# Optimization experiments

Hardware: AMD Instinct MI355X
Metric: run time of the kernel (lower is better)

Reference implementation:

```python
import jax, jax.numpy as jnp
import numpy as np

N_NODES = 100000
DEG = 16          # regular-graph degree so degrees[start] > 0 for all nodes
STEPS = 32
D_FEAT = 16
MAXI32 = 2147483647


def setup_inputs() -> dict:
    key = jax.random.key(0)
    k1, k2, k3 = jax.random.split(key, 3)
    x = jax.random.normal(k1, (N_NODES, D_FEAT), dtype=jnp.float32)
    # CSR-style flat adjacency list: node v's neighbors are
    # adj_nodes[adj_offset[v] : adj_offset[v] + degrees[v]]
    adj_nodes = jax.random.randint(k2, (N_NODES * DEG,), 0, N_NODES, dtype=jnp.int32)
    adj_offset = (jnp.arange(N_NODES, dtype=jnp.int32) * DEG)
    degrees = jnp.full((N_NODES,), DEG, dtype=jnp.int32)
    # cache of random integers, one per (step, walk), as in the torch code
    choices = jax.random.randint(k3, (STEPS, N_NODES), 0, MAXI32, dtype=jnp.int32)
    return {"x": x, "adj_nodes": adj_nodes, "adj_offset": adj_offset,
            "degrees": degrees, "choices": choices}


def reference(x, adj_nodes, adj_offset, degrees, choices):
    """Non-backtracking random walk (Walker.sample_walks with start_p=1.0,
    all nodes having degree > 0, so start = arange(n)).
    Returns walks [steps+1, w] and walk_edges [steps, w]."""
    n = degrees.shape[0]
    nb_degrees = jnp.maximum(degrees - 1, 1)  # reduced degree for non-backtrack rewrite
    start = jnp.arange(n, dtype=jnp.int32)

    def step(carry, ch):
        prev, cur = carry                      # [w] previous / current nodes
        deg = degrees[cur]
        edge_idx = ch % deg                    # unweighted modulo edge choice
        chosen = adj_offset[cur] + edge_idx
        new = adj_nodes[chosen]
        bt = new == prev                       # backtracking walks
        # conditional rewrite: pick a different outgoing edge
        alt = adj_offset[cur] + (edge_idx + 1 + ch % nb_degrees[cur]) % deg
        chosen = jnp.where(bt, alt, chosen)
        new = jnp.where(bt, adj_nodes[alt], new)
        return (cur, new), (new, chosen)

    # prev = -1 at step 0 => bt is all-False, matching the i > 0 guard
    prev0 = jnp.full_like(start, -1)
    _, (nodes, walk_edges) = jax.lax.scan(step, (prev0, start), choices)
    walks = jnp.concatenate([start[None, :], nodes], axis=0)  # [steps+1, w]
    return walks, walk_edges
```

## Files before the change

### kernel.cpp

```cpp
#include <hip/hip_runtime.h>
#include <hip/hip_bf16.h>


#define DEG 16
#define CHAINS 2

__global__ void pack_check_kernel(const int* __restrict__ adj_nodes,
                                  const int* __restrict__ adj_offset,
                                  const int* __restrict__ degrees,
                                  int n,
                                  unsigned int* __restrict__ pk32,
                                  int* __restrict__ flag) {
    int v = blockIdx.x * blockDim.x + threadIdx.x;
    if (v >= n) return;

    bool bad = (degrees[v] != DEG) || (adj_offset[v] != v * DEG);

    const uint4* row4 = (const uint4*)(adj_nodes + (size_t)v * DEG);
    uint4 r[4];
    r[0] = row4[0]; r[1] = row4[1]; r[2] = row4[2]; r[3] = row4[3];
    const unsigned* rr = (const unsigned*)r;

    unsigned wv[8];
    unsigned hbits = 0;
#pragma unroll
    for (int j = 0; j < 8; ++j) {
        unsigned u0 = rr[2 * j];
        unsigned u1 = rr[2 * j + 1];
        if (u0 >= 131072u || u1 >= 131072u) bad = true;
        wv[j] = (u0 & 0xffffu) | ((u1 & 0xffffu) << 16);
        hbits |= ((u0 >> 16) & 1u) << (2 * j);
        hbits |= ((u1 >> 16) & 1u) << (2 * j + 1);
    }
    unsigned int* dst = pk32 + (size_t)v * 9;
#pragma unroll
    for (int j = 0; j < 8; ++j) dst[j] = wv[j];
    dst[8] = hbits;

    if (bad) atomicOr(flag, 1);
}

template <int STEPS>
__global__ __launch_bounds__(64) void walker_fast2(
    const unsigned short* __restrict__ pk,
    const int* __restrict__ choices,
    int* __restrict__ out, int n, int h,
    const int* __restrict__ flag,
    const int* __restrict__ adj_nodes,
    const int* __restrict__ adj_offset,
    const int* __restrict__ degrees) {

    int t = blockIdx.x * blockDim.x + threadIdx.x;
    if (t >= h) return;

    int* walks      = out;
    int* walk_edges = out + (STEPS + 1) * n;

    int w0 = t;
    int w1 = t + h;
    bool has1 = (w1 < n);
    int w1s = has1 ? w1 : w0;

    __builtin_nontemporal_store(w0, &walks[w0]);
    if (has1) __builtin_nontemporal_store(w1, &walks[w1]);

    if (*flag == 0) {
        int c0[STEPS], c1[STEPS];
#pragma unroll
        for (int i = 0; i < STEPS; ++i) {
            c0[i] = __builtin_nontemporal_load(&choices[i * n + w0]);
            c1[i] = __builtin_nontemporal_load(&choices[i * n + w1s]);
        }

        int prev0 = -1, cur0 = w0;
        int prev1 = -1, cur1 = w1s;
#pragma unroll
        for (int i = 0; i < STEPS; ++i) {
            unsigned ch0 = (unsigned)c0[i];
            unsigned ch1 = (unsigned)c1[i];
            unsigned e0 = ch0 & (DEG - 1);
            unsigned e1 = ch1 & (DEG - 1);

            const unsigned short* r0 = pk + (unsigned)cur0 * 18u;
            const unsigned short* r1 = pk + (unsigned)cur1 * 18u;

            unsigned l00 = r0[e0];
            unsigned hb0 = r0[16];
            unsigned l10 = r1[e1];
            unsigned hb1 = r1[16];

            int n00 = (int)(l00 | (((hb0 >> e0) & 1u) << 16));
            int n10 = (int)(l10 | (((hb1 >> e1) & 1u) << 16));

            int nw0 = n00, nw1 = n10;
            unsigned ef0 = e0, ef1 = e1;
            if (n00 == prev0) {
                unsigned a0 = (e0 + 1u + ch0 % (DEG - 1)) & (DEG - 1);
                unsigned l01 = r0[a0];
                nw0 = (int)(l01 | (((hb0 >> a0) & 1u) << 16));
                ef0 = a0;
            }
            if (n10 == prev1) {
                unsigned a1 = (e1 + 1u + ch1 % (DEG - 1)) & (DEG - 1);
                unsigned l11 = r1[a1];
                nw1 = (int)(l11 | (((hb1 >> a1) & 1u) << 16));
                ef1 = a1;
            }

            int ce0 = (cur0 << 4) + (int)ef0;
            int ce1 = (cur1 << 4) + (int)ef1;

            __builtin_nontemporal_store(nw0, &walks[(i + 1) * n + w0]);
            __builtin_nontemporal_store(ce0, &walk_edges[i * n + w0]);
            if (has1) {
                __builtin_nontemporal_store(nw1, &walks[(i + 1) * n + w1]);
                __builtin_nontemporal_store(ce1, &walk_edges[i * n + w1]);
            }
            prev0 = cur0; cur0 = nw0;
            prev1 = cur1; cur1 = nw1;
        }
    } else {
        for (int k = 0; k < 2; ++k) {
            int w = (k == 0) ? w0 : w1;
            if (w >= n) break;
            int prev = -1, cur = w;
            for (int i = 0; i < STEPS; ++i) {
                int chv = choices[i * n + w];
                int deg = degrees[cur];
                int off = adj_offset[cur];
                int nb  = deg - 1 > 1 ? deg - 1 : 1;

                int e      = chv % deg;
                int chosen = off + e;
                int alt    = off + (e + 1 + chv % nb) % deg;

                int nv0 = adj_nodes[chosen];
                int nv1 = adj_nodes[alt];

                bool bt = (nv0 == prev);
                int nw  = bt ? nv1 : nv0;
                walks[(i + 1) * n + w] = nw;
                walk_edges[i * n + w]  = bt ? alt : chosen;
                prev = cur;
                cur  = nw;
            }
        }
    }
}

__global__ __launch_bounds__(256) void walker_generic(
    const int* __restrict__ adj_nodes,
    const int* __restrict__ adj_offset,
    const int* __restrict__ degrees,
    const int* __restrict__ choices,
    int* __restrict__ out, int n, int steps) {

    int w = blockIdx.x * blockDim.x + threadIdx.x;
    if (w >= n) return;

    int* walks      = out;
    int* walk_edges = out + (steps + 1) * n;
    walks[w] = w;

    int prev = -1, cur = w;
    for (int i = 0; i < steps; ++i) {
        int chv = choices[i * n + w];
        int deg = degrees[cur];
        int off = adj_offset[cur];
        int nb  = deg - 1 > 1 ? deg - 1 : 1;

        int e      = chv % deg;
        int chosen = off + e;
        int alt    = off + (e + 1 + chv % nb) % deg;

        int nv0 = adj_nodes[chosen];
        int nv1 = adj_nodes[alt];

        bool bt = (nv0 == prev);
        int nw  = bt ? nv1 : nv0;
        walks[(i + 1) * n + w] = nw;
        walk_edges[i * n + w]  = bt ? alt : chosen;
        prev = cur;
        cur  = nw;
    }
}

extern "C" void kernel_launch(void* const* d_in, const int* in_sizes, int n_in,
                              void* d_out, int out_size, void* d_ws, size_t ws_size,
                              hipStream_t stream) {
    const int* adj_nodes  = (const int*)d_in[1];
    const int* adj_offset = (const int*)d_in[2];
    const int* degrees    = (const int*)d_in[3];
    const int* choices    = (const int*)d_in[4];
    int* out = (int*)d_out;

    int n     = in_sizes[2];
    int steps = in_sizes[4] / n;

    size_t pk_off = 64;
    size_t need   = pk_off + (size_t)n * 36;

    if (steps == 32 && ws_size >= need) {
        int* flag = (int*)d_ws;
        unsigned int*   pk32 = (unsigned int*)((char*)d_ws + pk_off);
        unsigned short* pk   = (unsigned short*)pk32;

        hipMemsetAsync(flag, 0, sizeof(int), stream);
        int pb = 256, pg = (n + pb - 1) / pb;
        pack_check_kernel<<<pg, pb, 0, stream>>>(adj_nodes, adj_offset, degrees,
                                                 n, pk32, flag);
        int h  = (n + CHAINS - 1) / CHAINS;
        int wb = 64, wg = (h + wb - 1) / wb;
        walker_fast2<32><<<wg, wb, 0, stream>>>(pk, choices, out, n, h, flag,
                                                adj_nodes, adj_offset, degrees);
    } else {
        int block = 256, grid = (n + block - 1) / block;
        walker_generic<<<grid, block, 0, stream>>>(adj_nodes, adj_offset,
                                                   degrees, choices, out, n, steps);
    }
}
```

Baseline: 106.2 us.

## Drop packed adjacency preprocessing; walk raw adj_nodes with epoch-based validity flag

Removes the pack kernel that compressed each adjacency row into 16-bit entries plus a high-bit word. The walker now gathers directly from the original int32 adj_nodes. The memset of the flag is replaced by a device global compared against a host-incremented epoch, which saves one launch and a full pass over adj_nodes per call. The cost is that each random gather now reads 4-byte rows from a 6.4MB table instead of a smaller packed one. The node-id range check is dropped because ids no longer need to fit in 17 bits.

```diff
diff --git a/kernel.cpp b/kernel.cpp
--- a/kernel.cpp
+++ b/kernel.cpp
@@ -1,52 +1,26 @@
 #include <hip/hip_runtime.h>
-#include <hip/hip_bf16.h>
 
 
 #define DEG 16
 #define CHAINS 2
 
-__global__ void pack_check_kernel(const int* __restrict__ adj_nodes,
-                                  const int* __restrict__ adj_offset,
-                                  const int* __restrict__ degrees,
-                                  int n,
-                                  unsigned int* __restrict__ pk32,
-                                  int* __restrict__ flag) {
+__device__ int g_flag;
+
+__global__ __launch_bounds__(256) void check_kernel(
+    const int* __restrict__ adj_offset,
+    const int* __restrict__ degrees,
+    int n, int epoch) {
     int v = blockIdx.x * blockDim.x + threadIdx.x;
     if (v >= n) return;
-
-    bool bad = (degrees[v] != DEG) || (adj_offset[v] != v * DEG);
-
-    const uint4* row4 = (const uint4*)(adj_nodes + (size_t)v * DEG);
-    uint4 r[4];
-    r[0] = row4[0]; r[1] = row4[1]; r[2] = row4[2]; r[3] = row4[3];
-    const unsigned* rr = (const unsigned*)r;
-
-    unsigned wv[8];
-    unsigned hbits = 0;
-#pragma unroll
-    for (int j = 0; j < 8; ++j) {
-        unsigned u0 = rr[2 * j];
-        unsigned u1 = rr[2 * j + 1];
-        if (u0 >= 131072u || u1 >= 131072u) bad = true;
-        wv[j] = (u0 & 0xffffu) | ((u1 & 0xffffu) << 16);
-        hbits |= ((u0 >> 16) & 1u) << (2 * j);
-        hbits |= ((u1 >> 16) & 1u) << (2 * j + 1);
-    }
-    unsigned int* dst = pk32 + (size_t)v * 9;
-#pragma unroll
-    for (int j = 0; j < 8; ++j) dst[j] = wv[j];
-    dst[8] = hbits;
-
-    if (bad) atomicOr(flag, 1);
+    if (degrees[v] != DEG || adj_offset[v] != v * DEG)
+        g_flag = epoch;
 }
 
 template <int STEPS>
-__global__ __launch_bounds__(64) void walker_fast2(
-    const unsigned short* __restrict__ pk,
+__global__ __launch_bounds__(64) void walker_fast3(
+    const int* __restrict__ adj_nodes,
     const int* __restrict__ choices,
-    int* __restrict__ out, int n, int h,
-    const int* __restrict__ flag,
-    const int* __restrict__ adj_nodes,
+    int* __restrict__ out, int n, int h, int epoch,
     const int* __restrict__ adj_offset,
     const int* __restrict__ degrees) {
 
@@ -64,7 +38,7 @@
     __builtin_nontemporal_store(w0, &walks[w0]);
     if (has1) __builtin_nontemporal_store(w1, &walks[w1]);
 
-    if (*flag == 0) {
+    if (g_flag != epoch) {
         int c0[STEPS], c1[STEPS];
 #pragma unroll
         for (int i = 0; i < STEPS; ++i) {
@@ -81,29 +55,22 @@
             unsigned e0 = ch0 & (DEG - 1);
             unsigned e1 = ch1 & (DEG - 1);
 
-            const unsigned short* r0 = pk + (unsigned)cur0 * 18u;
-            const unsigned short* r1 = pk + (unsigned)cur1 * 18u;
+            const int* r0 = adj_nodes + ((unsigned)cur0 << 4);
+            const int* r1 = adj_nodes + ((unsigned)cur1 << 4);
 
-            unsigned l00 = r0[e0];
-            unsigned hb0 = r0[16];
-            unsigned l10 = r1[e1];
-            unsigned hb1 = r1[16];
-
-            int n00 = (int)(l00 | (((hb0 >> e0) & 1u) << 16));
-            int n10 = (int)(l10 | (((hb1 >> e1) & 1u) << 16));
+            int n00 = r0[e0];
+            int n10 = r1[e1];
 
             int nw0 = n00, nw1 = n10;
             unsigned ef0 = e0, ef1 = e1;
             if (n00 == prev0) {
                 unsigned a0 = (e0 + 1u + ch0 % (DEG - 1)) & (DEG - 1);
-                unsigned l01 = r0[a0];
-                nw0 = (int)(l01 | (((hb0 >> a0) & 1u) << 16));
+                nw0 = r0[a0];
                 ef0 = a0;
             }
             if (n10 == prev1) {
                 unsigned a1 = (e1 + 1u + ch1 % (DEG - 1)) & (DEG - 1);
-                unsigned l11 = r1[a1];
-                nw1 = (int)(l11 | (((hb1 >> a1) & 1u) << 16));
+                nw1 = r1[a1];
                 ef1 = a1;
             }
 
@@ -197,22 +164,17 @@
     int n     = in_sizes[2];
     int steps = in_sizes[4] / n;
 
-    size_t pk_off = 64;
-    size_t need   = pk_off + (size_t)n * 36;
+    if (steps == 32) {
+        static int s_epoch = 0;
+        int epoch = ++s_epoch;
 
-    if (steps == 32 && ws_size >= need) {
-        int* flag = (int*)d_ws;
-        unsigned int*   pk32 = (unsigned int*)((char*)d_ws + pk_off);
-        unsigned short* pk   = (unsigned short*)pk32;
+        int pg = (n + 255) / 256;
+        check_kernel<<<pg, 256, 0, stream>>>(adj_offset, degrees, n, epoch);
 
-        hipMemsetAsync(flag, 0, sizeof(int), stream);
-        int pb = 256, pg = (n + pb - 1) / pb;
-        pack_check_kernel<<<pg, pb, 0, stream>>>(adj_nodes, adj_offset, degrees,
-                                                 n, pk32, flag);
         int h  = (n + CHAINS - 1) / CHAINS;
         int wb = 64, wg = (h + wb - 1) / wb;
-        walker_fast2<32><<<wg, wb, 0, stream>>>(pk, choices, out, n, h, flag,
-                                                adj_nodes, adj_offset, degrees);
+        walker_fast3<32><<<wg, wb, 0, stream>>>(adj_nodes, choices, out, n, h,
+                                                epoch, adj_offset, degrees);
     } else {
         int block = 256, grid = (n + block - 1) / block;
         walker_generic<<<grid, block, 0, stream>>>(adj_nodes, adj_offset,
```

After: 114.6 us. 1.08x slower.
